# Kernel optimization log

Hardware: AMD Instinct MI355X
Metric: run time of the kernel (lower is better)

The kernel has to match this reference:

```python
import jax, jax.numpy as jnp
import numpy as np
import math

B, D, NH, NS, NT = 16, 256, 512, 8, 32
NV = NS * NT          # 256 prediction variables
L, H, A = 4, 8, 64    # attention layers, heads, head dim
HA = H * A            # 512
M = 512               # mlp_dim
R = 128               # resolution
EPS = 1e-5


def setup_inputs() -> dict:
    key = jax.random.key(0)
    ks = jax.random.split(key, 32)
    s = 0.02
    inp = {
        'hist_encoded': jax.random.normal(ks[0], (B, NH, D), jnp.float32),
        'hist_true_u': jax.random.uniform(ks[1], (B, NH), jnp.float32),
        'pred_encoded': jax.random.normal(ks[2], (B, NV, D), jnp.float32),
        'pred_true_u': jax.random.uniform(ks[3], (B, NV), jnp.float32),
        # dimension shifting layer
        'ds_w': jax.random.normal(ks[4], (D, HA), jnp.float32) * s,
        'ds_b': jnp.zeros((HA,), jnp.float32),
        # per-layer, per-head key/value creators: Linear(D+1 -> A)
        'key_w': jax.random.normal(ks[5], (L, H, D + 1, A), jnp.float32) * s,
        'key_b': jnp.zeros((L, H, A), jnp.float32),
        'val_w': jax.random.normal(ks[6], (L, H, D + 1, A), jnp.float32) * s,
        'val_b': jnp.zeros((L, H, A), jnp.float32),
        # layer norms
        'ln1_g': jnp.ones((L, HA), jnp.float32),
        'ln1_b': jnp.zeros((L, HA), jnp.float32),
        'ln2_g': jnp.ones((L, HA), jnp.float32),
        'ln2_b': jnp.zeros((L, HA), jnp.float32),
        # feed-forward (mlp_layers=2): HA->M, M->M, M->HA
        'ff_w1': jax.random.normal(ks[7], (L, HA, M), jnp.float32) * s,
        'ff_b1': jnp.zeros((L, M), jnp.float32),
        'ff_w2': jax.random.normal(ks[8], (L, M, M), jnp.float32) * s,
        'ff_b2': jnp.zeros((L, M), jnp.float32),
        'ff_w3': jax.random.normal(ks[9], (L, M, HA), jnp.float32) * s,
        'ff_b3': jnp.zeros((L, HA), jnp.float32),
        # dist extractor
        'de_w': jax.random.normal(ks[10], (HA, R), jnp.float32) * s,
        'de_b': jnp.zeros((R,), jnp.float32),
        'num_series': NS,
        'num_timesteps': NT,
    }
    return inp


def _ln(x, g, b):
    m = x.mean(-1, keepdims=True)
    v = ((x - m) ** 2).mean(-1, keepdims=True)
    return g * (x - m) / jnp.sqrt(v + EPS) + b


def _forward(hist_encoded, hist_true_u, pred_encoded, pred_true_u,
             ds_w, ds_b, key_w, key_b, val_w, val_b,
             ln1_g, ln1_b, ln2_g, ln2_b,
             ff_w1, ff_b1, ff_w2, ff_b2, ff_w3, ff_b3,
             de_w, de_b):
    Bm, NVm, Dm = pred_encoded.shape
    NHm = hist_encoded.shape[1]
    Lm, Hm, _, Am = key_w.shape
    W = NHm + NVm
    # identity permutation in the source loss() -> no-op
    att = pred_encoded @ ds_w + ds_b  # [B, NV, HA]
    # key/value inputs: [hist||u ; pred||u] -> [B, W, D+1]
    ki = jnp.concatenate([
        jnp.concatenate([hist_encoded, hist_true_u[:, :, None]], axis=2),
        jnp.concatenate([pred_encoded, pred_true_u[:, :, None]], axis=2)], axis=1)
    keys = jnp.einsum('bwd,lhda->lbhwa', ki, key_w) + key_b[:, None, :, None, :]
    vals = jnp.einsum('bwd,lhda->lbhwa', ki, val_w) + val_b[:, None, :, None, :]
    # flipped-triangular mask: position w is masked iff w >= NH + v
    mask = jnp.arange(W)[None, :] >= (NHm + jnp.arange(NVm)[:, None])  # [NV, W]
    scale = Am ** (-0.5)
    for l in range(Lm):
        avh = att.reshape(Bm, NVm, Hm, Am)
        prod = jnp.einsum('bvhi,bhwi->bhvw', avh, keys[l])  # [B,H,NV,W]
        prod = jnp.where(mask, -jnp.inf, prod) * scale
        w = jax.nn.softmax(prod, axis=-1)
        a = jnp.einsum('bhvw,bhwj->bvhj', w, vals[l]).reshape(Bm, NVm, Hm * Am)
        att = _ln(att + a, ln1_g[l], ln1_b[l])
        ff = jnp.maximum(att @ ff_w1[l] + ff_b1[l], 0.0)
        ff = jnp.maximum(ff @ ff_w2[l] + ff_b2[l], 0.0)
        ff = ff @ ff_w3[l] + ff_b3[l]
        att = _ln(att + ff, ln2_g[l], ln2_b[l])
    res = de_w.shape[-1]
    target = jnp.clip(jnp.floor(pred_true_u[:, 1:] * res).astype(jnp.int32), 0, res - 1)
    logits = (att @ de_w + de_b)[:, 1:, :]
    lp = math.log(res) + jax.nn.log_softmax(logits, axis=2)
    lp = jnp.take_along_axis(lp, target[:, :, None], axis=2)[:, :, 0]
    return -lp.sum(axis=1)  # [B]


def reference(hist_encoded, hist_true_u, pred_encoded, pred_true_u,
              ds_w, ds_b, key_w, key_b, val_w, val_b,
              ln1_g, ln1_b, ln2_g, ln2_b,
              ff_w1, ff_b1, ff_w2, ff_b2, ff_w3, ff_b3,
              de_w, de_b, num_series, num_timesteps):
    assert pred_encoded.shape[1] == num_series * num_timesteps
    return _forward(hist_encoded, hist_true_u, pred_encoded, pred_true_u,
                    ds_w, ds_b, key_w, key_b, val_w, val_b,
                    ln1_g, ln1_b, ln2_g, ln2_b,
                    ff_w1, ff_b1, ff_w2, ff_b2, ff_w3, ff_b3,
                    de_w, de_b)
```

## Files before the change

kernel.cpp:

```cpp
#include <hip/hip_runtime.h>

constexpr int kB = 16, kD = 256, kNH = 512, kNV = 256, kW = 768;
constexpr int kL = 4, kH = 8, kA = 64, kHA = 512, kM = 512, kR = 128;
constexpr int kKP = 288;
constexpr int kRows = kB * kNV;

typedef __bf16 bf16x8 __attribute__((ext_vector_type(8)));
typedef __bf16 bf16x4 __attribute__((ext_vector_type(4)));
typedef float f32x4 __attribute__((ext_vector_type(4)));

__device__ inline void load_lds16(const __bf16* g, __bf16* l) {
  __builtin_amdgcn_global_load_lds(
      (const __attribute__((address_space(1))) void*)g,
      (__attribute__((address_space(3))) void*)l, 16, 0, 0);
}

constexpr int kP1 = kB * kW * kKP;
constexpr int kP2 = 4096 * kKP;
constexpr int kP3 = 12 * 512 * 512;
constexpr int kP4 = 200704;
constexpr int kP5 = 16;
constexpr int kPT = kP1 + kP2 + kP3 + kP4 + kP5;

__global__ void prep_kernel(const float* __restrict__ hist,
                            const float* __restrict__ hist_u,
                            const float* __restrict__ pred,
                            const float* __restrict__ pred_u,
                            const float* __restrict__ kw,
                            const float* __restrict__ vw,
                            const float* __restrict__ w1,
                            const float* __restrict__ w2,
                            const float* __restrict__ w3,
                            const float* __restrict__ ds_w,
                            const float* __restrict__ de_w,
                            const float* __restrict__ key_b,
                            const float* __restrict__ val_b,
                            __bf16* __restrict__ ki,
                            __bf16* __restrict__ kvwt,
                            __bf16* __restrict__ ffwt,
                            __bf16* __restrict__ ds_wt,
                            __bf16* __restrict__ de_wt,
                            float* __restrict__ kvb,
                            float* __restrict__ outz) {
  int i = blockIdx.x * 256 + threadIdx.x;
  if (i < kP1) {
    int d = i % kKP;
    int bw = i / kKP;
    int w = bw % kW;
    int b = bw / kW;
    float v = 0.f;
    if (d < 257) {
      if (w < kNH)
        v = (d < kD) ? hist[((size_t)b * kNH + w) * kD + d] : hist_u[b * kNH + w];
      else {
        int p = w - kNH;
        v = (d < kD) ? pred[((size_t)b * kNV + p) * kD + d] : pred_u[b * kNV + p];
      }
    }
    ki[i] = (__bf16)v;
  } else if (i < kP1 + kP2) {
    int j = i - kP1;
    int d = j % kKP;
    int c = j / kKP;
    float v = 0.f;
    if (d < 257) {
      bool isv = c >= 2048;
      int cc = isv ? c - 2048 : c;
      int l = cc >> 9, rest = cc & 511;
      int h = rest >> 6, a = rest & 63;
      size_t src = (((size_t)l * kH + h) * 257 + d) * kA + a;
      v = isv ? vw[src] : kw[src];
    }
    kvwt[j] = (__bf16)v;
  } else if (i < kP1 + kP2 + kP3) {
    int j = i - kP1 - kP2;
    int k = j & 511;
    int n = (j >> 9) & 511;
    int mat = j >> 18;
    int l = mat / 3, which = mat % 3;
    const float* src = which == 0 ? w1 : which == 1 ? w2 : w3;
    ffwt[j] = (__bf16)src[((size_t)l * 512 + k) * 512 + n];
  } else if (i < kP1 + kP2 + kP3 + kP4) {
    int j = i - kP1 - kP2 - kP3;
    if (j < 131072) {
      int n = j >> 8, k = j & 255;
      ds_wt[j] = (__bf16)ds_w[k * 512 + n];
    } else if (j < 196608) {
      int jj = j - 131072;
      int n = jj >> 9, k = jj & 511;
      de_wt[jj] = (__bf16)de_w[k * 128 + n];
    } else {
      int c = j - 196608;
      bool isv = c >= 2048;
      int cc = isv ? c - 2048 : c;
      int l = cc >> 9, rest = cc & 511;
      kvb[c] = isv ? val_b[l * 512 + rest] : key_b[l * 512 + rest];
    }
  } else if (i < kPT) {
    outz[i - kP1 - kP2 - kP3 - kP4] = 0.f;
  }
}

template <int BN, int OMODE, bool RELU, bool KIMAP, bool BIASROW>
__device__ __forceinline__ void gemm_core(
    int bxv, int byv, const __bf16* __restrict__ A,
    const __bf16* __restrict__ Bt, const float* __restrict__ bias,
    void* __restrict__ Cout, __bf16* __restrict__ Cout2, int K, int lda,
    int ldc, __bf16* As, __bf16* Bs) {
  constexpr int JN = BN / 32;
  constexpr int BROWS = BN / 4;
  const int t = threadIdx.x;
  const int wid = t >> 6;
  const int lane = t & 63;
  const int bm = byv * 128;
  const int bn = bxv * BN;
  const int wm = (wid >> 1) * 64;
  const int wn = (wid & 1) * (BN / 2);
  const int sr = lane >> 2, sc = lane & 3;
  const int skey = (sr >> 1) & 3;
  const int abase = KIMAP ? ((bm >> 8) * 768 + 512 + (bm & 255)) : bm;
  const __bf16* Ag = A + (size_t)(abase + wid * 32 + sr) * lda + (sc ^ skey) * 8;
  const __bf16* Bg = Bt + (size_t)(bn + wid * BROWS + sr) * K + (sc ^ skey) * 8;
  __bf16* AsW = As + (wid * 32) * 32;
  __bf16* BsW = Bs + (wid * BROWS) * 32;

  f32x4 acc[4][JN] = {};
  const int q = lane >> 4, mr = lane & 15;
  const int rkey = (mr >> 1) & 3;
  for (int k0 = 0; k0 < K; k0 += 32) {
    if (k0) __syncthreads();
    load_lds16(Ag + k0, AsW);
    load_lds16(Ag + (size_t)16 * lda + k0, AsW + 16 * 32);
    load_lds16(Bg + k0, BsW);
    if (BN == 128) load_lds16(Bg + (size_t)16 * K + k0, BsW + 16 * 32);
    __syncthreads();
    bf16x8 af[4], bfr[JN];
#pragma unroll
    for (int i = 0; i < 4; ++i)
      af[i] = *(const bf16x8*)(As + (wm + i * 16 + mr) * 32 + (q ^ rkey) * 8);
#pragma unroll
    for (int j = 0; j < JN; ++j)
      bfr[j] = *(const bf16x8*)(Bs + (wn + j * 16 + mr) * 32 + (q ^ rkey) * 8);
#pragma unroll
    for (int i = 0; i < 4; ++i)
#pragma unroll
      for (int j = 0; j < JN; ++j)
        acc[i][j] = __builtin_amdgcn_mfma_f32_16x16x32_bf16(af[i], bfr[j],
                                                            acc[i][j], 0, 0, 0);
  }
#pragma unroll
  for (int j = 0; j < JN; ++j) {
    int col = bn + wn + j * 16 + mr;
    float bscol = BIASROW ? 0.f : bias[col];
#pragma unroll
    for (int i = 0; i < 4; ++i) {
      int row0 = bm + wm + i * 16 + q * 4;
#pragma unroll
      for (int r = 0; r < 4; ++r) {
        float v = acc[i][j][r] + (BIASROW ? bias[row0 + r] : bscol);
        if (RELU) v = fmaxf(v, 0.f);
        size_t idx = (size_t)(row0 + r) * ldc + col;
        if (OMODE == 0) {
          ((float*)Cout)[idx] = v;
        } else if (OMODE == 1) {
          ((__bf16*)Cout)[idx] = (__bf16)v;
        } else {
          ((float*)Cout)[idx] = v;
          Cout2[idx] = (__bf16)v;
        }
      }
    }
  }
}

__global__ __launch_bounds__(256) void gemm3_kernel(
    const __bf16* __restrict__ ki, const __bf16* __restrict__ ds_wt,
    const float* __restrict__ ds_b, float* __restrict__ att,
    __bf16* __restrict__ att_bf, const __bf16* __restrict__ kv_wt,
    const float* __restrict__ kvb, __bf16* __restrict__ kvs_k,
    __bf16* __restrict__ vT) {
  __shared__ __bf16 smem[8192];
  __bf16* As = smem;
  __bf16* Bs = smem + 4096;
  int bid = blockIdx.x;
  if (bid < 256) {
    gemm_core<64, 2, false, true, false>(bid & 7, bid >> 3, ki, ds_wt, ds_b,
                                         att, att_bf, 256, kKP, 512, As, Bs);
  } else if (bid < 1792) {
    int b2 = bid - 256;
    gemm_core<128, 1, false, false, false>(b2 & 15, b2 >> 4, ki, kv_wt, kvb,
                                           kvs_k, nullptr, kKP, kKP, 2048, As,
                                           Bs);
  } else {
    int b3 = bid - 1792;
    gemm_core<128, 1, false, false, true>(b3 % 96, b3 / 96,
                                          kv_wt + (size_t)2048 * kKP, ki,
                                          kvb + 2048, vT, nullptr, kKP, kKP,
                                          12288, As, Bs);
  }
}

template <bool RELU>
__global__ __launch_bounds__(256) void gemm_ff_kernel(
    const __bf16* __restrict__ A, const __bf16* __restrict__ Bt,
    const float* __restrict__ bias, __bf16* __restrict__ Cout) {
  __shared__ __bf16 smem[6144];
  gemm_core<64, 1, RELU, false, false>(blockIdx.x, blockIdx.y, A, Bt, bias,
                                       Cout, nullptr, 512, 512, 512, smem,
                                       smem + 4096);
}

__global__ __launch_bounds__(256) void attn_mfma_kernel(
    const __bf16* __restrict__ attbf, const __bf16* __restrict__ kvs_k,
    const __bf16* __restrict__ vT, __bf16* __restrict__ outbf, int l) {
  const int b = blockIdx.z, h = blockIdx.y, qt = blockIdx.x;
  __shared__ __bf16 Ks[64 * 72];
  __shared__ __bf16 Vt[64 * 72];
  __shared__ __bf16 Ps[64 * 72];
  const int t = threadIdx.x;
  const int w = t >> 6, lane = t & 63;
  const int quad = lane >> 4, mr = lane & 15;
  bf16x8 aq[2];
  {
    const __bf16* qp = attbf + ((size_t)(b * kNV + qt * 64 + w * 16 + mr) * kHA +
                                h * kA + quad * 8);
    aq[0] = *(const bf16x8*)qp;
    aq[1] = *(const bf16x8*)(qp + 32);
  }
  f32x4 o[4] = {};
  float m_ = -1e30f, l_ = 0.f;
  const int cmax = kNH + qt * 64;
  const int pr = t >> 2, pc = t & 3;
  const __bf16* kbase = kvs_k + ((size_t)(b * kW + pr) * 2048 + l * 512 + h * kA);
  const __bf16* vbase = vT + (size_t)(l * 512 + h * kA + pr) * 12288 + b * kW;
  bf16x8 kc0, kc1, vc0, vc1;
  kc0 = *(const bf16x8*)(kbase + pc * 8);
  kc1 = *(const bf16x8*)(kbase + pc * 8 + 32);
  vc0 = *(const bf16x8*)(vbase + pc * 16);
  vc1 = *(const bf16x8*)(vbase + pc * 16 + 8);
  for (int c0 = 0; c0 <= cmax; c0 += 64) {
    __syncthreads();
    *(bf16x8*)&Ks[pr * 72 + pc * 8] = kc0;
    *(bf16x8*)&Ks[pr * 72 + pc * 8 + 32] = kc1;
    *(bf16x8*)&Vt[pr * 72 + pc * 16] = vc0;
    *(bf16x8*)&Vt[pr * 72 + pc * 16 + 8] = vc1;
    __syncthreads();
    if (c0 + 64 <= cmax) {
      const __bf16* kp = kbase + (size_t)(c0 + 64) * 2048;
      const __bf16* vp = vbase + c0 + 64;
      kc0 = *(const bf16x8*)(kp + pc * 8);
      kc1 = *(const bf16x8*)(kp + pc * 8 + 32);
      vc0 = *(const bf16x8*)(vp + pc * 16);
      vc1 = *(const bf16x8*)(vp + pc * 16 + 8);
    }
    f32x4 s[4];
#pragma unroll
    for (int j = 0; j < 4; ++j) {
      bf16x8 ak0 = *(const bf16x8*)&Ks[(j * 16 + mr) * 72 + quad * 8];
      bf16x8 ak1 = *(const bf16x8*)&Ks[(j * 16 + mr) * 72 + quad * 8 + 32];
      f32x4 z = {};
      z = __builtin_amdgcn_mfma_f32_16x16x32_bf16(ak0, aq[0], z, 0, 0, 0);
      z = __builtin_amdgcn_mfma_f32_16x16x32_bf16(ak1, aq[1], z, 0, 0, 0);
      s[j] = z;
    }
    const int lim = cmax - c0;
    float sv[16], mx = -1e30f;
#pragma unroll
    for (int j = 0; j < 4; ++j)
#pragma unroll
      for (int r = 0; r < 4; ++r) {
        int p = j * 16 + quad * 4 + r;
        float x = (p < lim + mr) ? s[j][r] * 0.125f : -1e30f;
        sv[j * 4 + r] = x;
        mx = fmaxf(mx, x);
      }
    mx = fmaxf(mx, __shfl_xor(mx, 16));
    mx = fmaxf(mx, __shfl_xor(mx, 32));
    float mnew = fmaxf(m_, mx);
    float corr = __expf(m_ - mnew);
    float rs = 0.f;
#pragma unroll
    for (int i = 0; i < 16; ++i) {
      sv[i] = __expf(sv[i] - mnew);
      rs += sv[i];
    }
    rs += __shfl_xor(rs, 16);
    rs += __shfl_xor(rs, 32);
    l_ = l_ * corr + rs;
    m_ = mnew;
#pragma unroll
    for (int j = 0; j < 4; ++j) {
      bf16x4 pk = {(__bf16)sv[j * 4 + 0], (__bf16)sv[j * 4 + 1],
                   (__bf16)sv[j * 4 + 2], (__bf16)sv[j * 4 + 3]};
      *(bf16x4*)&Ps[(w * 16 + mr) * 72 + j * 16 + quad * 4] = pk;
    }
#pragma unroll
    for (int r = 0; r < 4; ++r) {
      float cr = __shfl(corr, quad * 4 + r);
#pragma unroll
      for (int j = 0; j < 4; ++j) o[j][r] *= cr;
    }
    bf16x8 ap0 = *(const bf16x8*)&Ps[(w * 16 + mr) * 72 + quad * 8];
    bf16x8 ap1 = *(const bf16x8*)&Ps[(w * 16 + mr) * 72 + quad * 8 + 32];
#pragma unroll
    for (int j = 0; j < 4; ++j) {
      bf16x8 b0 = *(const bf16x8*)&Vt[(j * 16 + mr) * 72 + quad * 8];
      bf16x8 b1 = *(const bf16x8*)&Vt[(j * 16 + mr) * 72 + quad * 8 + 32];
      o[j] = __builtin_amdgcn_mfma_f32_16x16x32_bf16(ap0, b0, o[j], 0, 0, 0);
      o[j] = __builtin_amdgcn_mfma_f32_16x16x32_bf16(ap1, b1, o[j], 0, 0, 0);
    }
  }
  float invl = 1.f / l_;
#pragma unroll
  for (int r = 0; r < 4; ++r) {
    float ir = __shfl(invl, quad * 4 + r);
    int row = b * kNV + qt * 64 + w * 16 + quad * 4 + r;
#pragma unroll
    for (int j = 0; j < 4; ++j)
      outbf[(size_t)row * kHA + h * kA + j * 16 + mr] = (__bf16)(o[j][r] * ir);
  }
}

__global__ __launch_bounds__(128) void add_ln_kernel(
    float* __restrict__ att, const __bf16* __restrict__ addbf,
    const float* __restrict__ g, const float* __restrict__ be,
    __bf16* __restrict__ attbf) {
  const int row = blockIdx.x;
  const int t = threadIdx.x;
  float4* ar = (float4*)(att + (size_t)row * kHA);
  bf16x4 dv = *(const bf16x4*)(addbf + (size_t)row * kHA + t * 4);
  float4 x = ar[t];
  x.x += (float)dv[0]; x.y += (float)dv[1];
  x.z += (float)dv[2]; x.w += (float)dv[3];
  float s = x.x + x.y + x.z + x.w;
  float sq = x.x * x.x + x.y * x.y + x.z * x.z + x.w * x.w;
  for (int o = 32; o; o >>= 1) {
    s += __shfl_xor(s, o);
    sq += __shfl_xor(sq, o);
  }
  __shared__ float red[4];
  if ((t & 63) == 0) { red[(t >> 6) * 2] = s; red[(t >> 6) * 2 + 1] = sq; }
  __syncthreads();
  float S = red[0] + red[2], Q = red[1] + red[3];
  float mean = S * (1.f / kHA);
  float inv = rsqrtf(Q * (1.f / kHA) - mean * mean + 1e-5f);
  float4 gv = ((const float4*)g)[t];
  float4 bv = ((const float4*)be)[t];
  float4 y;
  y.x = gv.x * (x.x - mean) * inv + bv.x;
  y.y = gv.y * (x.y - mean) * inv + bv.y;
  y.z = gv.z * (x.z - mean) * inv + bv.z;
  y.w = gv.w * (x.w - mean) * inv + bv.w;
  ar[t] = y;
  bf16x4 yb = {(__bf16)y.x, (__bf16)y.y, (__bf16)y.z, (__bf16)y.w};
  *(bf16x4*)(attbf + (size_t)row * kHA + t * 4) = yb;
}

__global__ __launch_bounds__(256) void de_loss_kernel(
    const __bf16* __restrict__ attbf, const __bf16* __restrict__ de_wt,
    const float* __restrict__ de_b, const float* __restrict__ pred_u,
    float* __restrict__ out) {
  const int blk = blockIdx.x;
  const int t = threadIdx.x;
  const int w = t >> 6, lane = t & 63, quad = lane >> 4, mr = lane & 15;
  const int row0 = blk * 64 + w * 16;
  f32x4 acc[8] = {};
  const __bf16* Ap = attbf + (size_t)(row0 + mr) * kHA + quad * 8;
#pragma unroll 4
  for (int k0 = 0; k0 < 512; k0 += 32) {
    bf16x8 a = *(const bf16x8*)(Ap + k0);
#pragma unroll
    for (int j = 0; j < 8; ++j) {
      bf16x8 bb =
          *(const bf16x8*)(de_wt + (size_t)(j * 16 + mr) * 512 + k0 + quad * 8);
      acc[j] = __builtin_amdgcn_mfma_f32_16x16x32_bf16(a, bb, acc[j], 0, 0, 0);
    }
  }
  float dbv[8];
#pragma unroll
  for (int j = 0; j < 8; ++j) dbv[j] = de_b[j * 16 + mr];
  float lpacc = 0.f;
#pragma unroll
  for (int r = 0; r < 4; ++r) {
    int row = row0 + quad * 4 + r;
    int v = row & 255;
    float lg[8], mx = -1e30f;
#pragma unroll
    for (int j = 0; j < 8; ++j) {
      lg[j] = acc[j][r] + dbv[j];
      mx = fmaxf(mx, lg[j]);
    }
    mx = fmaxf(mx, __shfl_xor(mx, 1));
    mx = fmaxf(mx, __shfl_xor(mx, 2));
    mx = fmaxf(mx, __shfl_xor(mx, 4));
    mx = fmaxf(mx, __shfl_xor(mx, 8));
    float se = 0.f;
#pragma unroll
    for (int j = 0; j < 8; ++j) se += __expf(lg[j] - mx);
    se += __shfl_xor(se, 1);
    se += __shfl_xor(se, 2);
    se += __shfl_xor(se, 4);
    se += __shfl_xor(se, 8);
    float lse = mx + __logf(se);
    float u = pred_u[(row >> 8) * 256 + v];
    int tgt = (int)floorf(u * 128.f);
    tgt = max(0, min(127, tgt));
    float cand = (mr == (tgt & 15)) ? lg[tgt >> 4] : 0.f;
    cand += __shfl_xor(cand, 1);
    cand += __shfl_xor(cand, 2);
    cand += __shfl_xor(cand, 4);
    cand += __shfl_xor(cand, 8);
    float lp = (v >= 1) ? (4.8520302639196171f + cand - lse) : 0.f;
    lpacc += lp;
  }
  lpacc += __shfl_xor(lpacc, 16);
  lpacc += __shfl_xor(lpacc, 32);
  __shared__ float red[4];
  if (lane == 0) red[w] = lpacc;
  __syncthreads();
  if (t == 0)
    atomicAdd(&out[blk >> 2], -(red[0] + red[1] + red[2] + red[3]));
}

extern "C" void kernel_launch(void* const* d_in, const int* in_sizes, int n_in,
                              void* d_out, int out_size, void* d_ws, size_t ws_size,
                              hipStream_t stream) {
  const float* hist   = (const float*)d_in[0];
  const float* hist_u = (const float*)d_in[1];
  const float* pred   = (const float*)d_in[2];
  const float* pred_u = (const float*)d_in[3];
  const float* ds_w   = (const float*)d_in[4];
  const float* ds_b   = (const float*)d_in[5];
  const float* key_w  = (const float*)d_in[6];
  const float* key_b  = (const float*)d_in[7];
  const float* val_w  = (const float*)d_in[8];
  const float* val_b  = (const float*)d_in[9];
  const float* ln1_g  = (const float*)d_in[10];
  const float* ln1_b  = (const float*)d_in[11];
  const float* ln2_g  = (const float*)d_in[12];
  const float* ln2_b  = (const float*)d_in[13];
  const float* ff_w1  = (const float*)d_in[14];
  const float* ff_b1  = (const float*)d_in[15];
  const float* ff_w2  = (const float*)d_in[16];
  const float* ff_b2  = (const float*)d_in[17];
  const float* ff_w3  = (const float*)d_in[18];
  const float* ff_b3  = (const float*)d_in[19];
  const float* de_w   = (const float*)d_in[20];
  const float* de_b   = (const float*)d_in[21];
  float* out = (float*)d_out;

  char* ws = (char*)d_ws;
  size_t off = 0;
  auto alloc = [&](size_t bytes) { char* p = ws + off; off += bytes; return p; };
  __bf16* ki_bf  = (__bf16*)alloc((size_t)kB * kW * kKP * 2);
  __bf16* kv_wt  = (__bf16*)alloc((size_t)4096 * kKP * 2);
  __bf16* ffw_t  = (__bf16*)alloc((size_t)12 * 512 * 512 * 2);
  __bf16* ds_wt  = (__bf16*)alloc((size_t)512 * 256 * 2);
  __bf16* de_wt  = (__bf16*)alloc((size_t)128 * 512 * 2);
  float*  kvb    = (float*)alloc((size_t)4096 * 4);
  __bf16* kvs_k  = (__bf16*)alloc((size_t)kB * kW * 2048 * 2);
  __bf16* vT     = (__bf16*)alloc((size_t)2048 * 12288 * 2);
  float*  att    = (float*)alloc((size_t)kRows * kHA * 4);
  __bf16* att_bf = (__bf16*)alloc((size_t)kRows * kHA * 2);
  __bf16* tmp_bf = (__bf16*)alloc((size_t)kRows * kHA * 2);
  __bf16* ff1_bf = (__bf16*)alloc((size_t)kRows * kM * 2);
  __bf16* ff2_bf = (__bf16*)alloc((size_t)kRows * kM * 2);

  prep_kernel<<<(kPT + 255) / 256, 256, 0, stream>>>(
      hist, hist_u, pred, pred_u, key_w, val_w, ff_w1, ff_w2, ff_w3, ds_w, de_w,
      key_b, val_b, ki_bf, kv_wt, ffw_t, ds_wt, de_wt, kvb, out);

  gemm3_kernel<<<3328, 256, 0, stream>>>(ki_bf, ds_wt, ds_b, att, att_bf, kv_wt,
                                         kvb, kvs_k, vT);

  for (int l = 0; l < kL; ++l) {
    attn_mfma_kernel<<<dim3(kNV / 64, kH, kB), 256, 0, stream>>>(
        att_bf, kvs_k, vT, tmp_bf, l);
    add_ln_kernel<<<kRows, 128, 0, stream>>>(att, tmp_bf, ln1_g + l * kHA,
                                             ln1_b + l * kHA, att_bf);
    gemm_ff_kernel<true><<<dim3(kM / 64, kRows / 128), 256, 0, stream>>>(
        att_bf, ffw_t + (size_t)(l * 3) * 262144, ff_b1 + l * kM, ff1_bf);
    gemm_ff_kernel<true><<<dim3(kM / 64, kRows / 128), 256, 0, stream>>>(
        ff1_bf, ffw_t + (size_t)(l * 3 + 1) * 262144, ff_b2 + l * kM, ff2_bf);
    gemm_ff_kernel<false><<<dim3(kHA / 64, kRows / 128), 256, 0, stream>>>(
        ff2_bf, ffw_t + (size_t)(l * 3 + 2) * 262144, ff_b3 + l * kHA, tmp_bf);
    add_ln_kernel<<<kRows, 128, 0, stream>>>(att, tmp_bf, ln2_g + l * kHA,
                                             ln2_b + l * kHA, att_bf);
  }
  de_loss_kernel<<<64, 256, 0, stream>>>(att_bf, de_wt, de_b, pred_u, out);
}
```

Baseline: 470.0 us.

## Fuse add-LayerNorm, three-layer MLP, and second LayerNorm into one kernel per layer

Replaces the per-layer sequence of two add+LayerNorm kernels and three FF GEMM kernels with a single kernel. Each block handles 16 rows and keeps the normalized input and intermediate activations in swizzled LDS. Weight fragments are read straight from global memory into MFMA operands. This removes four launches per layer and the global round-trips of the intermediate activations. In exchange, each block re-reads all 1.5 MB of weights per layer without LDS tiling, and the large LDS footprint of about 48 KB per block may limit occupancy.

```diff
diff --git a/kernel.cpp b/kernel.cpp
--- a/kernel.cpp
+++ b/kernel.cpp
@@ -200,14 +200,169 @@
   }
 }
 
+__device__ __forceinline__ void ff_gemm_acc(const __bf16* __restrict__ Als,
+                                            const __bf16* __restrict__ Wt,
+                                            int w, int quad, int mr,
+                                            f32x4 acc[4]) {
+  const __bf16* B0 = Wt + (size_t)(w * 64 + mr) * 512 + quad * 8;
+  const __bf16* Ab = Als + mr * 512;
+  const int sw = mr & 7;
+#pragma unroll 4
+  for (int ks = 0; ks < 16; ++ks) {
+    bf16x8 af = *(const bf16x8*)(Ab + (((ks * 4 + quad) ^ sw) << 3));
+#pragma unroll
+    for (int nt = 0; nt < 4; ++nt) {
+      bf16x8 bfv = *(const bf16x8*)(B0 + nt * 8192 + ks * 32);
+      acc[nt] = __builtin_amdgcn_mfma_f32_16x16x32_bf16(af, bfv, acc[nt], 0, 0, 0);
+    }
+  }
+}
+
 template <bool RELU>
-__global__ __launch_bounds__(256) void gemm_ff_kernel(
-    const __bf16* __restrict__ A, const __bf16* __restrict__ Bt,
-    const float* __restrict__ bias, __bf16* __restrict__ Cout) {
-  __shared__ __bf16 smem[6144];
-  gemm_core<64, 1, RELU, false, false>(blockIdx.x, blockIdx.y, A, Bt, bias,
-                                       Cout, nullptr, 512, 512, 512, smem,
-                                       smem + 4096);
+__device__ __forceinline__ void ff_epi_lds(const f32x4 acc[4],
+                                           const float* __restrict__ bias,
+                                           int w, int quad, int mr,
+                                           __bf16* __restrict__ hout) {
+#pragma unroll
+  for (int nt = 0; nt < 4; ++nt) {
+    const int col = w * 64 + nt * 16 + mr;
+    const float bv = bias[col];
+#pragma unroll
+    for (int r = 0; r < 4; ++r) {
+      const int row = quad * 4 + r;
+      float v = acc[nt][r] + bv;
+      if (RELU) v = fmaxf(v, 0.f);
+      hout[row * 512 + (((col >> 3) ^ (row & 7)) << 3) + (mr & 7)] = (__bf16)v;
+    }
+  }
+}
+
+__global__ __launch_bounds__(512, 4) void ff_fused_kernel(
+    float* __restrict__ att, const __bf16* __restrict__ addbf,
+    const float* __restrict__ g1, const float* __restrict__ b1g,
+    const float* __restrict__ g2, const float* __restrict__ b2g,
+    const __bf16* __restrict__ Wt, const float* __restrict__ fb1,
+    const float* __restrict__ fb2, const float* __restrict__ fb3,
+    __bf16* __restrict__ attbf) {
+  __shared__ __attribute__((aligned(16))) float y32[16 * 512];
+  __shared__ __attribute__((aligned(16))) __bf16 ybf[16 * 512];
+  __shared__ __attribute__((aligned(16))) __bf16 h1[16 * 512];
+  __shared__ float redS[8][16], redQ[8][16];
+  const int t = threadIdx.x, w = t >> 6, lane = t & 63;
+  const int quad = lane >> 4, mr = lane & 15;
+  const int r0 = blockIdx.x * 16;
+  {
+    const int c0 = lane * 8;
+    const float4 ga = *(const float4*)(g1 + c0);
+    const float4 gb = *(const float4*)(g1 + c0 + 4);
+    const float4 ba = *(const float4*)(b1g + c0);
+    const float4 bb = *(const float4*)(b1g + c0 + 4);
+#pragma unroll
+    for (int rr = 0; rr < 2; ++rr) {
+      const int row = w * 2 + rr;
+      const size_t base = (size_t)(r0 + row) * 512 + c0;
+      float4 a0 = *(const float4*)(att + base);
+      float4 a1 = *(const float4*)(att + base + 4);
+      bf16x8 d = *(const bf16x8*)(addbf + base);
+      float x[8] = {a0.x + (float)d[0], a0.y + (float)d[1], a0.z + (float)d[2],
+                    a0.w + (float)d[3], a1.x + (float)d[4], a1.y + (float)d[5],
+                    a1.z + (float)d[6], a1.w + (float)d[7]};
+      float s = 0.f, q = 0.f;
+#pragma unroll
+      for (int j = 0; j < 8; ++j) { s += x[j]; q += x[j] * x[j]; }
+#pragma unroll
+      for (int o = 1; o < 64; o <<= 1) {
+        s += __shfl_xor(s, o);
+        q += __shfl_xor(q, o);
+      }
+      const float mean = s * (1.f / 512.f);
+      const float inv = rsqrtf(q * (1.f / 512.f) - mean * mean + 1e-5f);
+      float y[8];
+      y[0] = ga.x * (x[0] - mean) * inv + ba.x;
+      y[1] = ga.y * (x[1] - mean) * inv + ba.y;
+      y[2] = ga.z * (x[2] - mean) * inv + ba.z;
+      y[3] = ga.w * (x[3] - mean) * inv + ba.w;
+      y[4] = gb.x * (x[4] - mean) * inv + bb.x;
+      y[5] = gb.y * (x[5] - mean) * inv + bb.y;
+      y[6] = gb.z * (x[6] - mean) * inv + bb.z;
+      y[7] = gb.w * (x[7] - mean) * inv + bb.w;
+      *(float4*)(y32 + row * 512 + c0) = (float4){y[0], y[1], y[2], y[3]};
+      *(float4*)(y32 + row * 512 + c0 + 4) = (float4){y[4], y[5], y[6], y[7]};
+      bf16x8 yv = {(__bf16)y[0], (__bf16)y[1], (__bf16)y[2], (__bf16)y[3],
+                   (__bf16)y[4], (__bf16)y[5], (__bf16)y[6], (__bf16)y[7]};
+      *(bf16x8*)(ybf + row * 512 + ((lane ^ (row & 7)) << 3)) = yv;
+    }
+  }
+  __syncthreads();
+  {
+    f32x4 acc[4] = {};
+    ff_gemm_acc(ybf, Wt, w, quad, mr, acc);
+    ff_epi_lds<true>(acc, fb1, w, quad, mr, h1);
+  }
+  __syncthreads();
+  {
+    f32x4 acc[4] = {};
+    ff_gemm_acc(h1, Wt + 262144, w, quad, mr, acc);
+    ff_epi_lds<true>(acc, fb2, w, quad, mr, ybf);
+  }
+  __syncthreads();
+  f32x4 acc[4] = {};
+  ff_gemm_acc(ybf, Wt + 524288, w, quad, mr, acc);
+  float x2v[4][4], ps[4] = {}, pq[4] = {};
+#pragma unroll
+  for (int nt = 0; nt < 4; ++nt) {
+    const int col = w * 64 + nt * 16 + mr;
+    const float bv = fb3[col];
+#pragma unroll
+    for (int r = 0; r < 4; ++r) {
+      const int row = quad * 4 + r;
+      const float v = acc[nt][r] + bv + y32[row * 512 + col];
+      x2v[nt][r] = v;
+      ps[r] += v;
+      pq[r] += v * v;
+    }
+  }
+#pragma unroll
+  for (int r = 0; r < 4; ++r)
+#pragma unroll
+    for (int o = 1; o < 16; o <<= 1) {
+      ps[r] += __shfl_xor(ps[r], o);
+      pq[r] += __shfl_xor(pq[r], o);
+    }
+  if (mr == 0) {
+#pragma unroll
+    for (int r = 0; r < 4; ++r) {
+      redS[w][quad * 4 + r] = ps[r];
+      redQ[w][quad * 4 + r] = pq[r];
+    }
+  }
+  __syncthreads();
+  float mean_[4], inv_[4];
+#pragma unroll
+  for (int r = 0; r < 4; ++r) {
+    const int row = quad * 4 + r;
+    float S = 0.f, Q = 0.f;
+#pragma unroll
+    for (int wv = 0; wv < 8; ++wv) {
+      S += redS[wv][row];
+      Q += redQ[wv][row];
+    }
+    mean_[r] = S * (1.f / 512.f);
+    inv_[r] = rsqrtf(Q * (1.f / 512.f) - mean_[r] * mean_[r] + 1e-5f);
+  }
+#pragma unroll
+  for (int nt = 0; nt < 4; ++nt) {
+    const int col = w * 64 + nt * 16 + mr;
+    const float gv = g2[col], bv = b2g[col];
+#pragma unroll
+    for (int r = 0; r < 4; ++r) {
+      const int row = quad * 4 + r;
+      const size_t idx = (size_t)(r0 + row) * 512 + col;
+      const float z = gv * (x2v[nt][r] - mean_[r]) * inv_[r] + bv;
+      att[idx] = z;
+      attbf[idx] = (__bf16)z;
+    }
+  }
 }
 
 __global__ __launch_bounds__(256) void attn_mfma_kernel(
@@ -319,41 +474,6 @@
     for (int j = 0; j < 4; ++j)
       outbf[(size_t)row * kHA + h * kA + j * 16 + mr] = (__bf16)(o[j][r] * ir);
   }
-}
-
-__global__ __launch_bounds__(128) void add_ln_kernel(
-    float* __restrict__ att, const __bf16* __restrict__ addbf,
-    const float* __restrict__ g, const float* __restrict__ be,
-    __bf16* __restrict__ attbf) {
-  const int row = blockIdx.x;
-  const int t = threadIdx.x;
-  float4* ar = (float4*)(att + (size_t)row * kHA);
-  bf16x4 dv = *(const bf16x4*)(addbf + (size_t)row * kHA + t * 4);
-  float4 x = ar[t];
-  x.x += (float)dv[0]; x.y += (float)dv[1];
-  x.z += (float)dv[2]; x.w += (float)dv[3];
-  float s = x.x + x.y + x.z + x.w;
-  float sq = x.x * x.x + x.y * x.y + x.z * x.z + x.w * x.w;
-  for (int o = 32; o; o >>= 1) {
-    s += __shfl_xor(s, o);
-    sq += __shfl_xor(sq, o);
-  }
-  __shared__ float red[4];
-  if ((t & 63) == 0) { red[(t >> 6) * 2] = s; red[(t >> 6) * 2 + 1] = sq; }
-  __syncthreads();
-  float S = red[0] + red[2], Q = red[1] + red[3];
-  float mean = S * (1.f / kHA);
-  float inv = rsqrtf(Q * (1.f / kHA) - mean * mean + 1e-5f);
-  float4 gv = ((const float4*)g)[t];
-  float4 bv = ((const float4*)be)[t];
-  float4 y;
-  y.x = gv.x * (x.x - mean) * inv + bv.x;
-  y.y = gv.y * (x.y - mean) * inv + bv.y;
-  y.z = gv.z * (x.z - mean) * inv + bv.z;
-  y.w = gv.w * (x.w - mean) * inv + bv.w;
-  ar[t] = y;
-  bf16x4 yb = {(__bf16)y.x, (__bf16)y.y, (__bf16)y.z, (__bf16)y.w};
-  *(bf16x4*)(attbf + (size_t)row * kHA + t * 4) = yb;
 }
 
 __global__ __launch_bounds__(256) void de_loss_kernel(
@@ -463,8 +583,6 @@
   float*  att    = (float*)alloc((size_t)kRows * kHA * 4);
   __bf16* att_bf = (__bf16*)alloc((size_t)kRows * kHA * 2);
   __bf16* tmp_bf = (__bf16*)alloc((size_t)kRows * kHA * 2);
-  __bf16* ff1_bf = (__bf16*)alloc((size_t)kRows * kM * 2);
-  __bf16* ff2_bf = (__bf16*)alloc((size_t)kRows * kM * 2);
 
   prep_kernel<<<(kPT + 255) / 256, 256, 0, stream>>>(
       hist, hist_u, pred, pred_u, key_w, val_w, ff_w1, ff_w2, ff_w3, ds_w, de_w,
@@ -476,16 +594,10 @@
   for (int l = 0; l < kL; ++l) {
     attn_mfma_kernel<<<dim3(kNV / 64, kH, kB), 256, 0, stream>>>(
         att_bf, kvs_k, vT, tmp_bf, l);
-    add_ln_kernel<<<kRows, 128, 0, stream>>>(att, tmp_bf, ln1_g + l * kHA,
-                                             ln1_b + l * kHA, att_bf);
-    gemm_ff_kernel<true><<<dim3(kM / 64, kRows / 128), 256, 0, stream>>>(
-        att_bf, ffw_t + (size_t)(l * 3) * 262144, ff_b1 + l * kM, ff1_bf);
-    gemm_ff_kernel<true><<<dim3(kM / 64, kRows / 128), 256, 0, stream>>>(
-        ff1_bf, ffw_t + (size_t)(l * 3 + 1) * 262144, ff_b2 + l * kM, ff2_bf);
-    gemm_ff_kernel<false><<<dim3(kHA / 64, kRows / 128), 256, 0, stream>>>(
-        ff2_bf, ffw_t + (size_t)(l * 3 + 2) * 262144, ff_b3 + l * kHA, tmp_bf);
-    add_ln_kernel<<<kRows, 128, 0, stream>>>(att, tmp_bf, ln2_g + l * kHA,
-                                             ln2_b + l * kHA, att_bf);
+    ff_fused_kernel<<<kRows / 16, 512, 0, stream>>>(
+        att, tmp_bf, ln1_g + l * kHA, ln1_b + l * kHA, ln2_g + l * kHA,
+        ln2_b + l * kHA, ffw_t + (size_t)(l * 3) * 262144, ff_b1 + l * kM,
+        ff_b2 + l * kM, ff_b3 + l * kHA, att_bf);
   }
   de_loss_kernel<<<64, 256, 0, stream>>>(att_bf, de_wt, de_b, pred_u, out);
 }
```

Result: slower. 499.1 us (+6.2%).
